# Kernel optimization log

Hardware: AMD Instinct MI355X
Metric: run time of the kernel (lower is better)

The kernel has to match this reference:

```python
import jax, jax.numpy as jnp
import numpy as np

N_NODES = 50000
N_EDGES = 800000
N_GRAPHS = 256
HEADS = 4
OUT_CH = 32
HIDDEN = HEADS * OUT_CH  # 128
NUM_LAYERS = 3
NEG_SLOPE = 0.2
BN_EPS = 1e-5


def setup_inputs() -> dict:
    key = jax.random.key(0)
    ks = jax.random.split(key, 12)
    x = jax.random.normal(ks[0], (N_NODES, HIDDEN), dtype=jnp.float32)
    edge_index = jax.random.randint(ks[1], (2, N_EDGES), 0, N_NODES, dtype=jnp.int64)
    batch = jnp.sort(jax.random.randint(ks[2], (N_NODES,), 0, N_GRAPHS, dtype=jnp.int64))
    s = 1.0 / np.sqrt(HIDDEN)
    W = jax.random.normal(ks[3], (NUM_LAYERS, HIDDEN, HIDDEN), dtype=jnp.float32) * s
    att_src = jax.random.normal(ks[4], (NUM_LAYERS, HEADS, OUT_CH), dtype=jnp.float32) * s
    att_dst = jax.random.normal(ks[5], (NUM_LAYERS, HEADS, OUT_CH), dtype=jnp.float32) * s
    bias = jnp.zeros((NUM_LAYERS, HIDDEN), dtype=jnp.float32)
    bn_gamma = jnp.ones((NUM_LAYERS, HIDDEN), dtype=jnp.float32)
    bn_beta = jnp.zeros((NUM_LAYERS, HIDDEN), dtype=jnp.float32)
    bn_mean = jnp.zeros((NUM_LAYERS, HIDDEN), dtype=jnp.float32)
    bn_var = jnp.ones((NUM_LAYERS, HIDDEN), dtype=jnp.float32)
    fc1_w = jax.random.normal(ks[6], (HIDDEN, HIDDEN // 2), dtype=jnp.float32) * s
    fc1_b = jnp.zeros((HIDDEN // 2,), dtype=jnp.float32)
    fc2_w = jax.random.normal(ks[7], (HIDDEN // 2, 10), dtype=jnp.float32) * (1.0 / np.sqrt(HIDDEN // 2))
    fc2_b = jnp.zeros((10,), dtype=jnp.float32)
    return {"x": x, "edge_index": edge_index, "batch": batch, "W": W,
            "att_src": att_src, "att_dst": att_dst, "bias": bias,
            "bn_gamma": bn_gamma, "bn_beta": bn_beta, "bn_mean": bn_mean,
            "bn_var": bn_var, "fc1_w": fc1_w, "fc1_b": fc1_b,
            "fc2_w": fc2_w, "fc2_b": fc2_b}


def _gat_layer(x, src, dst, W, a_src, a_dst, b):
    n = x.shape[0]
    h = (x @ W).reshape(n, HEADS, OUT_CH)                       # [N,H,C]
    alpha_s = jnp.einsum('nhc,hc->nh', h, a_src)                # [N,H]
    alpha_d = jnp.einsum('nhc,hc->nh', h, a_dst)                # [N,H]
    score = jax.nn.leaky_relu(alpha_s[src] + alpha_d[dst], NEG_SLOPE)  # [E,H]
    # segment softmax over destination node (self-loops guarantee nonempty segments)
    m = jax.lax.stop_gradient(jax.ops.segment_max(score, dst, num_segments=n))
    e = jnp.exp(score - m[dst])
    denom = jax.ops.segment_sum(e, dst, num_segments=n)
    alpha = e / denom[dst]                                      # [E,H]
    msg = h[src] * alpha[:, :, None]                            # [E,H,C]
    out = jax.ops.segment_sum(msg, dst, num_segments=n)         # [N,H,C]
    return out.reshape(n, HEADS * OUT_CH) + b


def reference(x, edge_index, batch, W, att_src, att_dst, bias,
              bn_gamma, bn_beta, bn_mean, bn_var,
              fc1_w, fc1_b, fc2_w, fc2_b):
    n = x.shape[0]
    loop = jnp.arange(n, dtype=edge_index.dtype)
    src = jnp.concatenate([edge_index[0], loop])  # add self-loops (PyG default)
    dst = jnp.concatenate([edge_index[1], loop])
    for i in range(NUM_LAYERS):
        x = _gat_layer(x, src, dst, W[i], att_src[i], att_dst[i], bias[i])
        x = (x - bn_mean[i]) * (bn_gamma[i] / jnp.sqrt(bn_var[i] + BN_EPS)) + bn_beta[i]
        x = jax.nn.elu(x)
    # global mean pool over graphs
    sums = jax.ops.segment_sum(x, batch, num_segments=N_GRAPHS)
    cnts = jax.ops.segment_sum(jnp.ones((n,), dtype=x.dtype), batch, num_segments=N_GRAPHS)
    pooled = sums / jnp.maximum(cnts, 1.0)[:, None]
    hmid = jax.nn.relu(pooled @ fc1_w + fc1_b)
    logits = hmid @ fc2_w + fc2_b
    return logits
```

## Files before the change

kernel.cpp:

```cpp
#include <hip/hip_runtime.h>
#include <hip/hip_fp16.h>
#include <math.h>

#define N_NODES 50000
#define N_EDGES 800000
#define E_TOTAL (N_EDGES + N_NODES)
#define N_GRAPHS 256
#define HEADS 4
#define OUT_CH 32
#define HIDDEN 128
#define NUM_LAYERS 3
#define NEG_SLOPE 0.2f
#define BN_EPS 1e-5f
#define NBLK_SCAN ((N_NODES + 255) / 256)


__global__ void zero_kernel(unsigned int* __restrict__ p, int n) {
    int i = blockIdx.x * blockDim.x + threadIdx.x;
    if (i < n) p[i] = 0u;
}


__global__ void hist_kernel(const int* __restrict__ dst, int* __restrict__ deg,
                            int* __restrict__ rank) {
    int e = blockIdx.x * blockDim.x + threadIdx.x;
    if (e >= E_TOTAL) return;
    int d = (e < N_EDGES) ? dst[e] : (e - N_EDGES);
    rank[e] = atomicAdd(&deg[d], 1);
}

__global__ __launch_bounds__(256) void scan1_kernel(const int* __restrict__ deg,
                                                    int* __restrict__ rowoff,
                                                    int* __restrict__ bsum, int n) {
    int i = blockIdx.x * 256 + threadIdx.x;
    int v = (i < n) ? deg[i] : 0;
    int lane = threadIdx.x & 63, wv = threadIdx.x >> 6;
    int s = v;
    for (int off = 1; off < 64; off <<= 1) {
        int u = __shfl_up(s, off);
        if (lane >= off) s += u;
    }
    __shared__ int wtot[4];
    if (lane == 63) wtot[wv] = s;
    __syncthreads();
    int add = 0;
    for (int w = 0; w < wv; ++w) add += wtot[w];
    s += add;
    if (i < n) rowoff[i + 1] = s;
    if (threadIdx.x == 255) bsum[blockIdx.x] = s;
}

__global__ __launch_bounds__(256) void scan2_kernel(int* __restrict__ bsum, int nb) {
    int t = threadIdx.x;
    int v = (t < nb) ? bsum[t] : 0;
    int lane = t & 63, wv = t >> 6;
    int s = v;
    for (int off = 1; off < 64; off <<= 1) {
        int u = __shfl_up(s, off);
        if (lane >= off) s += u;
    }
    __shared__ int wtot[4];
    if (lane == 63) wtot[wv] = s;
    __syncthreads();
    int add = 0;
    for (int w = 0; w < wv; ++w) add += wtot[w];
    s += add;
    if (t < nb) bsum[t] = s - v;
}

__global__ __launch_bounds__(256) void scan3_kernel(const int* __restrict__ bsum,
                                                    int* __restrict__ rowoff, int n) {
    int i = blockIdx.x * 256 + threadIdx.x;
    if (i == 0) rowoff[0] = 0;
    if (i < n) rowoff[i + 1] += bsum[blockIdx.x];
}

__global__ void scatter_kernel(const int* __restrict__ src, const int* __restrict__ dst,
                               const int* __restrict__ rowoff, const int* __restrict__ rank,
                               int2* __restrict__ edgebuf) {
    int e = blockIdx.x * blockDim.x + threadIdx.x;
    if (e >= E_TOTAL) return;
    int s, d;
    if (e < N_EDGES) { s = src[e]; d = dst[e]; }
    else             { s = e - N_EDGES; d = s; }
    int pos = rowoff[d] + rank[e];
    edgebuf[pos] = make_int2(s, d);
}


__global__ __launch_bounds__(256) void gemm_xw(const float* __restrict__ X,
                                               const float* __restrict__ W,
                                               const float* __restrict__ att_src,
                                               const float* __restrict__ att_dst,
                                               __half* __restrict__ Hh,
                                               float* __restrict__ as4,
                                               float* __restrict__ ad4, int n) {
    __shared__ float xst[32][36];
    __shared__ float ws[32][128];
    const int row0 = blockIdx.x * 32;
    const int cg = threadIdx.x & 31;
    const int rg = threadIdx.x >> 5;
    float acc[4][4];
#pragma unroll
    for (int r = 0; r < 4; ++r)
#pragma unroll
        for (int j = 0; j < 4; ++j) acc[r][j] = 0.f;

    for (int k0 = 0; k0 < 128; k0 += 32) {
        {
            int r = threadIdx.x >> 3;
            int kk = (threadIdx.x & 7) * 4;
            int swz = (kk >> 2) & 7;
            int cswz = (((r >> 2) ^ swz) << 2) | (r & 3);
            int gr = row0 + r;
            float4 v = make_float4(0.f, 0.f, 0.f, 0.f);
            if (gr < n) v = *reinterpret_cast<const float4*>(&X[gr * 128 + k0 + kk]);
            xst[kk + 0][cswz] = v.x; xst[kk + 1][cswz] = v.y;
            xst[kk + 2][cswz] = v.z; xst[kk + 3][cswz] = v.w;
        }
        for (int i = threadIdx.x; i < 32 * 128 / 4; i += 256) {
            int p = i * 4;
            int kk = p >> 7, cc = p & 127;
            *reinterpret_cast<float4*>(&ws[kk][cc]) =
                *reinterpret_cast<const float4*>(&W[(k0 + kk) * 128 + cc]);
        }
        __syncthreads();
#pragma unroll
        for (int kk = 0; kk < 32; ++kk) {
            const int swz = (kk >> 2) & 7;
            float4 wv = *reinterpret_cast<const float4*>(&ws[kk][cg * 4]);
            float4 xv = *reinterpret_cast<const float4*>(&xst[kk][((rg ^ swz) << 2)]);
            acc[0][0] += xv.x * wv.x; acc[0][1] += xv.x * wv.y; acc[0][2] += xv.x * wv.z; acc[0][3] += xv.x * wv.w;
            acc[1][0] += xv.y * wv.x; acc[1][1] += xv.y * wv.y; acc[1][2] += xv.y * wv.z; acc[1][3] += xv.y * wv.w;
            acc[2][0] += xv.z * wv.x; acc[2][1] += xv.z * wv.y; acc[2][2] += xv.z * wv.z; acc[2][3] += xv.z * wv.w;
            acc[3][0] += xv.w * wv.x; acc[3][1] += xv.w * wv.y; acc[3][2] += xv.w * wv.z; acc[3][3] += xv.w * wv.w;
        }
        __syncthreads();
    }

#pragma unroll
    for (int r = 0; r < 4; ++r) {
        int gr = row0 + rg * 4 + r;
        if (gr < n) {
            __half2 ab = __floats2half2_rn(acc[r][0], acc[r][1]);
            __half2 cd = __floats2half2_rn(acc[r][2], acc[r][3]);
            uint2 u;
            u.x = *reinterpret_cast<unsigned*>(&ab);
            u.y = *reinterpret_cast<unsigned*>(&cd);
            *reinterpret_cast<uint2*>(&Hh[(size_t)gr * 128 + cg * 4]) = u;
        }
    }

    const int h = cg >> 3;
    const int co = (cg & 7) * 4;
    float4 asw = *reinterpret_cast<const float4*>(att_src + h * OUT_CH + co);
    float4 adw = *reinterpret_cast<const float4*>(att_dst + h * OUT_CH + co);
#pragma unroll
    for (int r = 0; r < 4; ++r) {
        float s = acc[r][0] * asw.x + acc[r][1] * asw.y + acc[r][2] * asw.z + acc[r][3] * asw.w;
        float d = acc[r][0] * adw.x + acc[r][1] * adw.y + acc[r][2] * adw.z + acc[r][3] * adw.w;
        s += __shfl_xor(s, 1); d += __shfl_xor(d, 1);
        s += __shfl_xor(s, 2); d += __shfl_xor(d, 2);
        s += __shfl_xor(s, 4); d += __shfl_xor(d, 4);
        if ((cg & 7) == 0) {
            int gr = row0 + rg * 4 + r;
            if (gr < n) {
                as4[gr * 4 + h] = s;
                ad4[gr * 4 + h] = d;
            }
        }
    }
}


__global__ __launch_bounds__(256) void escore_kernel(const int2* __restrict__ edgebuf,
                                                     const float* __restrict__ as4,
                                                     const float* __restrict__ ad4,
                                                     float* __restrict__ esc) {
    int j = blockIdx.x * blockDim.x + threadIdx.x;
    if (j >= E_TOTAL) return;
    int2 ed = edgebuf[j];
    float4 a = *reinterpret_cast<const float4*>(&as4[ed.x * 4]);
    float4 b = *reinterpret_cast<const float4*>(&ad4[ed.y * 4]);
    float x0 = a.x + b.x, x1 = a.y + b.y, x2 = a.z + b.z, x3 = a.w + b.w;
    x0 = x0 > 0.f ? x0 : x0 * NEG_SLOPE;
    x1 = x1 > 0.f ? x1 : x1 * NEG_SLOPE;
    x2 = x2 > 0.f ? x2 : x2 * NEG_SLOPE;
    x3 = x3 > 0.f ? x3 : x3 * NEG_SLOPE;
    float4 e = make_float4(__expf(x0), __expf(x1), __expf(x2), __expf(x3));
    *reinterpret_cast<float4*>(&esc[(size_t)j * 4]) = e;
}


template <int USE_ESC>
__global__ __launch_bounds__(256) void aggregate_kernel(
    const __half2* __restrict__ Hh2, const float* __restrict__ as4, const float* __restrict__ ad4,
    const float* __restrict__ esc,
    const int* __restrict__ rowoff, const int2* __restrict__ edgebuf,
    const float* __restrict__ bias, const float* __restrict__ gamma, const float* __restrict__ beta,
    const float* __restrict__ mean, const float* __restrict__ var,
    float* __restrict__ Xout, int n) {
    int wid = (blockIdx.x * blockDim.x + threadIdx.x) >> 6;
    if (wid >= n) return;
    int lane = threadIdx.x & 63;
    int hd = lane >> 4;
    int c = lane * 2;

    float adv = USE_ESC ? 0.f : ad4[wid * 4 + hd];

    int jbeg = rowoff[wid], jend = rowoff[wid + 1];

    float s = 0.f, ax = 0.f, ay = 0.f;

    for (int base = jbeg; base < jend; base += 64) {
        int myj = base + lane;
        int mysrc = (myj < jend) ? edgebuf[myj].x : 0;
        int cnt = min(64, jend - base);
        int t = 0;
        if (USE_ESC) {
#pragma unroll 1
            for (; t + 8 <= cnt; t += 8) {
                int s0 = __shfl(mysrc, t + 0);
                int s1 = __shfl(mysrc, t + 1);
                int s2 = __shfl(mysrc, t + 2);
                int s3 = __shfl(mysrc, t + 3);
                int s4 = __shfl(mysrc, t + 4);
                int s5 = __shfl(mysrc, t + 5);
                int s6 = __shfl(mysrc, t + 6);
                int s7 = __shfl(mysrc, t + 7);
                float e0 = esc[(size_t)(base + t + 0) * 4 + hd];
                float e1 = esc[(size_t)(base + t + 1) * 4 + hd];
                float e2 = esc[(size_t)(base + t + 2) * 4 + hd];
                float e3 = esc[(size_t)(base + t + 3) * 4 + hd];
                float e4 = esc[(size_t)(base + t + 4) * 4 + hd];
                float e5 = esc[(size_t)(base + t + 5) * 4 + hd];
                float e6 = esc[(size_t)(base + t + 6) * 4 + hd];
                float e7 = esc[(size_t)(base + t + 7) * 4 + hd];
                float2 h0 = __half22float2(Hh2[(size_t)s0 * 64 + lane]);
                float2 h1 = __half22float2(Hh2[(size_t)s1 * 64 + lane]);
                float2 h2 = __half22float2(Hh2[(size_t)s2 * 64 + lane]);
                float2 h3 = __half22float2(Hh2[(size_t)s3 * 64 + lane]);
                float2 h4 = __half22float2(Hh2[(size_t)s4 * 64 + lane]);
                float2 h5 = __half22float2(Hh2[(size_t)s5 * 64 + lane]);
                float2 h6 = __half22float2(Hh2[(size_t)s6 * 64 + lane]);
                float2 h7 = __half22float2(Hh2[(size_t)s7 * 64 + lane]);
                s  += ((e0 + e1) + (e2 + e3)) + ((e4 + e5) + (e6 + e7));
                ax += e0 * h0.x + e1 * h1.x + e2 * h2.x + e3 * h3.x
                    + e4 * h4.x + e5 * h5.x + e6 * h6.x + e7 * h7.x;
                ay += e0 * h0.y + e1 * h1.y + e2 * h2.y + e3 * h3.y
                    + e4 * h4.y + e5 * h5.y + e6 * h6.y + e7 * h7.y;
            }
        }
        for (; t < cnt; ++t) {
            int src = __shfl(mysrc, t);
            float e;
            if (USE_ESC) {
                e = esc[(size_t)(base + t) * 4 + hd];
            } else {
                float sc = as4[src * 4 + hd] + adv;
                sc = sc > 0.f ? sc : sc * NEG_SLOPE;
                e = __expf(sc);
            }
            float2 hv = __half22float2(Hh2[(size_t)src * 64 + lane]);
            s += e;
            ax += e * hv.x;
            ay += e * hv.y;
        }
    }

    float inv = 1.f / s;
    float v0 = ax * inv + bias[c];
    float v1 = ay * inv + bias[c + 1];
    v0 = (v0 - mean[c])     * (gamma[c]     * rsqrtf(var[c]     + BN_EPS)) + beta[c];
    v1 = (v1 - mean[c + 1]) * (gamma[c + 1] * rsqrtf(var[c + 1] + BN_EPS)) + beta[c + 1];
    v0 = v0 > 0.f ? v0 : expm1f(v0);
    v1 = v1 > 0.f ? v1 : expm1f(v1);
    float2 o = make_float2(v0, v1);
    *reinterpret_cast<float2*>(&Xout[(size_t)wid * HIDDEN + c]) = o;
}


__global__ __launch_bounds__(1024) void pool_fc_kernel(
    const float* __restrict__ X, const int* __restrict__ batch,
    const float* __restrict__ fc1w, const float* __restrict__ fc1b,
    const float* __restrict__ fc2w, const float* __restrict__ fc2b,
    float* __restrict__ out) {
    int g = blockIdx.x;
    int tid = threadIdx.x;
    int cg = (tid & 31) * 4;
    int rg = tid >> 5;

    int lo = 0, hi = N_NODES;
    while (lo < hi) { int mid = (lo + hi) >> 1; if (batch[mid] < g) lo = mid + 1; else hi = mid; }
    int lo2 = lo, hi2 = N_NODES;
    while (lo2 < hi2) { int mid = (lo2 + hi2) >> 1; if (batch[mid] < g + 1) lo2 = mid + 1; else hi2 = mid; }

    float ax = 0.f, ay = 0.f, az = 0.f, aw = 0.f;
    for (int i = lo + rg; i < lo2; i += 32) {
        float4 v = *reinterpret_cast<const float4*>(&X[(size_t)i * HIDDEN + cg]);
        ax += v.x; ay += v.y; az += v.z; aw += v.w;
    }

    __shared__ float red[32][132];
    red[rg][cg + 0] = ax; red[rg][cg + 1] = ay;
    red[rg][cg + 2] = az; red[rg][cg + 3] = aw;
    __syncthreads();
#pragma unroll
    for (int step = 16; step >= 1; step >>= 1) {
        if (rg < step) {
            red[rg][cg + 0] += red[rg + step][cg + 0];
            red[rg][cg + 1] += red[rg + step][cg + 1];
            red[rg][cg + 2] += red[rg + step][cg + 2];
            red[rg][cg + 3] += red[rg + step][cg + 3];
        }
        __syncthreads();
    }

    __shared__ float pooled[HIDDEN];
    __shared__ float hmid[64];
    if (rg == 0) {
        float inv = 1.f / fmaxf((float)(lo2 - lo), 1.0f);
        pooled[cg + 0] = red[0][cg + 0] * inv;
        pooled[cg + 1] = red[0][cg + 1] * inv;
        pooled[cg + 2] = red[0][cg + 2] * inv;
        pooled[cg + 3] = red[0][cg + 3] * inv;
    }
    __syncthreads();
    if (tid < 64) {
        float a = fc1b[tid];
#pragma unroll 8
        for (int k = 0; k < 128; ++k) a += pooled[k] * fc1w[k * 64 + tid];
        hmid[tid] = fmaxf(a, 0.f);
    }
    __syncthreads();
    if (tid < 10) {
        float a = fc2b[tid];
#pragma unroll 8
        for (int k = 0; k < 64; ++k) a += hmid[k] * fc2w[k * 10 + tid];
        out[g * 10 + tid] = a;
    }
}


static inline size_t align_up(size_t x, size_t a) { return (x + a - 1) & ~(a - 1); }

extern "C" void kernel_launch(void* const* d_in, const int* in_sizes, int n_in,
                              void* d_out, int out_size, void* d_ws, size_t ws_size,
                              hipStream_t stream) {
    const float* x        = (const float*)d_in[0];
    const int*   eidx     = (const int*)d_in[1];
    const int*   batch    = (const int*)d_in[2];
    const float* W        = (const float*)d_in[3];
    const float* att_src  = (const float*)d_in[4];
    const float* att_dst  = (const float*)d_in[5];
    const float* bias     = (const float*)d_in[6];
    const float* bn_gamma = (const float*)d_in[7];
    const float* bn_beta  = (const float*)d_in[8];
    const float* bn_mean  = (const float*)d_in[9];
    const float* bn_var   = (const float*)d_in[10];
    const float* fc1w     = (const float*)d_in[11];
    const float* fc1b     = (const float*)d_in[12];
    const float* fc2w     = (const float*)d_in[13];
    const float* fc2b     = (const float*)d_in[14];
    float* out = (float*)d_out;

    const int* src = eidx;
    const int* dst = eidx + N_EDGES;

    char* p = (char*)d_ws;
    size_t off = 0;
    auto alloc = [&](size_t bytes) {
        size_t o = off;
        off = align_up(off + bytes, 256);
        return (void*)(p + o);
    };
    __half* Hh     = (__half*)alloc((size_t)N_NODES * HIDDEN * 2);
    float* Xbuf    = (float*)alloc((size_t)N_NODES * HIDDEN * 4);
    float* as4     = (float*)alloc((size_t)N_NODES * HEADS * 4);
    float* ad4     = (float*)alloc((size_t)N_NODES * HEADS * 4);
    int*   deg     = (int*)alloc((size_t)N_NODES * 4);
    int*   rowoff  = (int*)alloc((size_t)(N_NODES + 1) * 4);
    int*   rank    = (int*)alloc((size_t)E_TOTAL * 4);
    int*   bsum    = (int*)alloc((size_t)NBLK_SCAN * 4);
    int2*  edgebuf = (int2*)alloc((size_t)E_TOTAL * 8);
    float* esc     = (float*)alloc((size_t)E_TOTAL * HEADS * 4);
    const bool use_esc = (off <= ws_size);
    (void)n_in; (void)in_sizes; (void)out_size;

    zero_kernel<<<(N_NODES + 255) / 256, 256, 0, stream>>>((unsigned int*)deg, N_NODES);

    hist_kernel<<<(E_TOTAL + 255) / 256, 256, 0, stream>>>(dst, deg, rank);
    scan1_kernel<<<NBLK_SCAN, 256, 0, stream>>>(deg, rowoff, bsum, N_NODES);
    scan2_kernel<<<1, 256, 0, stream>>>(bsum, NBLK_SCAN);
    scan3_kernel<<<NBLK_SCAN, 256, 0, stream>>>(bsum, rowoff, N_NODES);
    scatter_kernel<<<(E_TOTAL + 255) / 256, 256, 0, stream>>>(src, dst, rowoff, rank, edgebuf);

    const float* xcur = x;
    for (int layer = 0; layer < NUM_LAYERS; ++layer) {
        const float* Wl  = W + (size_t)layer * HIDDEN * HIDDEN;
        const float* asl = att_src + (size_t)layer * HEADS * OUT_CH;
        const float* adl = att_dst + (size_t)layer * HEADS * OUT_CH;
        const float* bl  = bias + (size_t)layer * HIDDEN;
        const float* gl  = bn_gamma + (size_t)layer * HIDDEN;
        const float* btl = bn_beta + (size_t)layer * HIDDEN;
        const float* ml  = bn_mean + (size_t)layer * HIDDEN;
        const float* vl  = bn_var + (size_t)layer * HIDDEN;

        gemm_xw<<<(N_NODES + 31) / 32, 256, 0, stream>>>(xcur, Wl, asl, adl, Hh, as4, ad4, N_NODES);
        if (use_esc) {
            escore_kernel<<<(E_TOTAL + 255) / 256, 256, 0, stream>>>(edgebuf, as4, ad4, esc);
            aggregate_kernel<1><<<(N_NODES * 64 + 255) / 256, 256, 0, stream>>>(
                (const __half2*)Hh, as4, ad4, esc, rowoff, edgebuf, bl, gl, btl, ml, vl, Xbuf, N_NODES);
        } else {
            aggregate_kernel<0><<<(N_NODES * 64 + 255) / 256, 256, 0, stream>>>(
                (const __half2*)Hh, as4, ad4, esc, rowoff, edgebuf, bl, gl, btl, ml, vl, Xbuf, N_NODES);
        }
        xcur = Xbuf;
    }

    pool_fc_kernel<<<N_GRAPHS, 1024, 0, stream>>>(xcur, batch, fc1w, fc1b, fc2w, fc2b, out);
}
```

Baseline: 402.3 us.

## Fuse edge score computation into aggregation and store only source indices in CSR

Removes the separate per-layer escore kernel and its E×4 float buffer. Attention weights are now recomputed inside the aggregation loop from gathered as4 values, using an 8-wide unrolled path. The CSR edge buffer shrinks from int2 (src,dst) to int src only. This cuts global memory traffic and one launch per layer, at the cost of an extra gather from as4 and more exp work inside the aggregation kernel.

```diff
diff --git a/kernel.cpp b/kernel.cpp
--- a/kernel.cpp
+++ b/kernel.cpp
@@ -77,14 +77,14 @@
 
 __global__ void scatter_kernel(const int* __restrict__ src, const int* __restrict__ dst,
                                const int* __restrict__ rowoff, const int* __restrict__ rank,
-                               int2* __restrict__ edgebuf) {
+                               int* __restrict__ col) {
     int e = blockIdx.x * blockDim.x + threadIdx.x;
     if (e >= E_TOTAL) return;
     int s, d;
     if (e < N_EDGES) { s = src[e]; d = dst[e]; }
     else             { s = e - N_EDGES; d = s; }
     int pos = rowoff[d] + rank[e];
-    edgebuf[pos] = make_int2(s, d);
+    col[pos] = s;
 }
 
 
@@ -173,30 +173,9 @@
 }
 
 
-__global__ __launch_bounds__(256) void escore_kernel(const int2* __restrict__ edgebuf,
-                                                     const float* __restrict__ as4,
-                                                     const float* __restrict__ ad4,
-                                                     float* __restrict__ esc) {
-    int j = blockIdx.x * blockDim.x + threadIdx.x;
-    if (j >= E_TOTAL) return;
-    int2 ed = edgebuf[j];
-    float4 a = *reinterpret_cast<const float4*>(&as4[ed.x * 4]);
-    float4 b = *reinterpret_cast<const float4*>(&ad4[ed.y * 4]);
-    float x0 = a.x + b.x, x1 = a.y + b.y, x2 = a.z + b.z, x3 = a.w + b.w;
-    x0 = x0 > 0.f ? x0 : x0 * NEG_SLOPE;
-    x1 = x1 > 0.f ? x1 : x1 * NEG_SLOPE;
-    x2 = x2 > 0.f ? x2 : x2 * NEG_SLOPE;
-    x3 = x3 > 0.f ? x3 : x3 * NEG_SLOPE;
-    float4 e = make_float4(__expf(x0), __expf(x1), __expf(x2), __expf(x3));
-    *reinterpret_cast<float4*>(&esc[(size_t)j * 4]) = e;
-}
-
-
-template <int USE_ESC>
 __global__ __launch_bounds__(256) void aggregate_kernel(
     const __half2* __restrict__ Hh2, const float* __restrict__ as4, const float* __restrict__ ad4,
-    const float* __restrict__ esc,
-    const int* __restrict__ rowoff, const int2* __restrict__ edgebuf,
+    const int* __restrict__ rowoff, const int* __restrict__ col,
     const float* __restrict__ bias, const float* __restrict__ gamma, const float* __restrict__ beta,
     const float* __restrict__ mean, const float* __restrict__ var,
     float* __restrict__ Xout, int n) {
@@ -206,7 +185,7 @@
     int hd = lane >> 4;
     int c = lane * 2;
 
-    float adv = USE_ESC ? 0.f : ad4[wid * 4 + hd];
+    float adv = ad4[wid * 4 + hd];
 
     int jbeg = rowoff[wid], jend = rowoff[wid + 1];
 
@@ -214,53 +193,62 @@
 
     for (int base = jbeg; base < jend; base += 64) {
         int myj = base + lane;
-        int mysrc = (myj < jend) ? edgebuf[myj].x : 0;
+        int mysrc = (myj < jend) ? col[myj] : 0;
         int cnt = min(64, jend - base);
         int t = 0;
-        if (USE_ESC) {
 #pragma unroll 1
-            for (; t + 8 <= cnt; t += 8) {
-                int s0 = __shfl(mysrc, t + 0);
-                int s1 = __shfl(mysrc, t + 1);
-                int s2 = __shfl(mysrc, t + 2);
-                int s3 = __shfl(mysrc, t + 3);
-                int s4 = __shfl(mysrc, t + 4);
-                int s5 = __shfl(mysrc, t + 5);
-                int s6 = __shfl(mysrc, t + 6);
-                int s7 = __shfl(mysrc, t + 7);
-                float e0 = esc[(size_t)(base + t + 0) * 4 + hd];
-                float e1 = esc[(size_t)(base + t + 1) * 4 + hd];
-                float e2 = esc[(size_t)(base + t + 2) * 4 + hd];
-                float e3 = esc[(size_t)(base + t + 3) * 4 + hd];
-                float e4 = esc[(size_t)(base + t + 4) * 4 + hd];
-                float e5 = esc[(size_t)(base + t + 5) * 4 + hd];
-                float e6 = esc[(size_t)(base + t + 6) * 4 + hd];
-                float e7 = esc[(size_t)(base + t + 7) * 4 + hd];
-                float2 h0 = __half22float2(Hh2[(size_t)s0 * 64 + lane]);
-                float2 h1 = __half22float2(Hh2[(size_t)s1 * 64 + lane]);
-                float2 h2 = __half22float2(Hh2[(size_t)s2 * 64 + lane]);
-                float2 h3 = __half22float2(Hh2[(size_t)s3 * 64 + lane]);
-                float2 h4 = __half22float2(Hh2[(size_t)s4 * 64 + lane]);
-                float2 h5 = __half22float2(Hh2[(size_t)s5 * 64 + lane]);
-                float2 h6 = __half22float2(Hh2[(size_t)s6 * 64 + lane]);
-                float2 h7 = __half22float2(Hh2[(size_t)s7 * 64 + lane]);
-                s  += ((e0 + e1) + (e2 + e3)) + ((e4 + e5) + (e6 + e7));
-                ax += e0 * h0.x + e1 * h1.x + e2 * h2.x + e3 * h3.x
-                    + e4 * h4.x + e5 * h5.x + e6 * h6.x + e7 * h7.x;
-                ay += e0 * h0.y + e1 * h1.y + e2 * h2.y + e3 * h3.y
-                    + e4 * h4.y + e5 * h5.y + e6 * h6.y + e7 * h7.y;
-            }
+        for (; t + 8 <= cnt; t += 8) {
+            int s0 = __shfl(mysrc, t + 0);
+            int s1 = __shfl(mysrc, t + 1);
+            int s2 = __shfl(mysrc, t + 2);
+            int s3 = __shfl(mysrc, t + 3);
+            int s4 = __shfl(mysrc, t + 4);
+            int s5 = __shfl(mysrc, t + 5);
+            int s6 = __shfl(mysrc, t + 6);
+            int s7 = __shfl(mysrc, t + 7);
+            float a0 = as4[s0 * 4 + hd];
+            float a1 = as4[s1 * 4 + hd];
+            float a2 = as4[s2 * 4 + hd];
+            float a3 = as4[s3 * 4 + hd];
+            float a4 = as4[s4 * 4 + hd];
+            float a5 = as4[s5 * 4 + hd];
+            float a6 = as4[s6 * 4 + hd];
+            float a7 = as4[s7 * 4 + hd];
+            float2 h0 = __half22float2(Hh2[(size_t)s0 * 64 + lane]);
+            float2 h1 = __half22float2(Hh2[(size_t)s1 * 64 + lane]);
+            float2 h2 = __half22float2(Hh2[(size_t)s2 * 64 + lane]);
+            float2 h3 = __half22float2(Hh2[(size_t)s3 * 64 + lane]);
+            float2 h4 = __half22float2(Hh2[(size_t)s4 * 64 + lane]);
+            float2 h5 = __half22float2(Hh2[(size_t)s5 * 64 + lane]);
+            float2 h6 = __half22float2(Hh2[(size_t)s6 * 64 + lane]);
+            float2 h7 = __half22float2(Hh2[(size_t)s7 * 64 + lane]);
+            float x0 = a0 + adv; x0 = x0 > 0.f ? x0 : x0 * NEG_SLOPE;
+            float x1 = a1 + adv; x1 = x1 > 0.f ? x1 : x1 * NEG_SLOPE;
+            float x2 = a2 + adv; x2 = x2 > 0.f ? x2 : x2 * NEG_SLOPE;
+            float x3 = a3 + adv; x3 = x3 > 0.f ? x3 : x3 * NEG_SLOPE;
+            float x4 = a4 + adv; x4 = x4 > 0.f ? x4 : x4 * NEG_SLOPE;
+            float x5 = a5 + adv; x5 = x5 > 0.f ? x5 : x5 * NEG_SLOPE;
+            float x6 = a6 + adv; x6 = x6 > 0.f ? x6 : x6 * NEG_SLOPE;
+            float x7 = a7 + adv; x7 = x7 > 0.f ? x7 : x7 * NEG_SLOPE;
+            float e0 = __expf(x0);
+            float e1 = __expf(x1);
+            float e2 = __expf(x2);
+            float e3 = __expf(x3);
+            float e4 = __expf(x4);
+            float e5 = __expf(x5);
+            float e6 = __expf(x6);
+            float e7 = __expf(x7);
+            s  += ((e0 + e1) + (e2 + e3)) + ((e4 + e5) + (e6 + e7));
+            ax += e0 * h0.x + e1 * h1.x + e2 * h2.x + e3 * h3.x
+                + e4 * h4.x + e5 * h5.x + e6 * h6.x + e7 * h7.x;
+            ay += e0 * h0.y + e1 * h1.y + e2 * h2.y + e3 * h3.y
+                + e4 * h4.y + e5 * h5.y + e6 * h6.y + e7 * h7.y;
         }
         for (; t < cnt; ++t) {
             int src = __shfl(mysrc, t);
-            float e;
-            if (USE_ESC) {
-                e = esc[(size_t)(base + t) * 4 + hd];
-            } else {
-                float sc = as4[src * 4 + hd] + adv;
-                sc = sc > 0.f ? sc : sc * NEG_SLOPE;
-                e = __expf(sc);
-            }
+            float sc = as4[src * 4 + hd] + adv;
+            sc = sc > 0.f ? sc : sc * NEG_SLOPE;
+            float e = __expf(sc);
             float2 hv = __half22float2(Hh2[(size_t)src * 64 + lane]);
             s += e;
             ax += e * hv.x;
@@ -382,10 +370,8 @@
     int*   rowoff  = (int*)alloc((size_t)(N_NODES + 1) * 4);
     int*   rank    = (int*)alloc((size_t)E_TOTAL * 4);
     int*   bsum    = (int*)alloc((size_t)NBLK_SCAN * 4);
-    int2*  edgebuf = (int2*)alloc((size_t)E_TOTAL * 8);
-    float* esc     = (float*)alloc((size_t)E_TOTAL * HEADS * 4);
-    const bool use_esc = (off <= ws_size);
-    (void)n_in; (void)in_sizes; (void)out_size;
+    int*   col     = (int*)alloc((size_t)E_TOTAL * 4);
+    (void)n_in; (void)in_sizes; (void)out_size; (void)ws_size;
 
     zero_kernel<<<(N_NODES + 255) / 256, 256, 0, stream>>>((unsigned int*)deg, N_NODES);
 
@@ -393,7 +379,7 @@
     scan1_kernel<<<NBLK_SCAN, 256, 0, stream>>>(deg, rowoff, bsum, N_NODES);
     scan2_kernel<<<1, 256, 0, stream>>>(bsum, NBLK_SCAN);
     scan3_kernel<<<NBLK_SCAN, 256, 0, stream>>>(bsum, rowoff, N_NODES);
-    scatter_kernel<<<(E_TOTAL + 255) / 256, 256, 0, stream>>>(src, dst, rowoff, rank, edgebuf);
+    scatter_kernel<<<(E_TOTAL + 255) / 256, 256, 0, stream>>>(src, dst, rowoff, rank, col);
 
     const float* xcur = x;
     for (int layer = 0; layer < NUM_LAYERS; ++layer) {
@@ -407,14 +393,8 @@
         const float* vl  = bn_var + (size_t)layer * HIDDEN;
 
         gemm_xw<<<(N_NODES + 31) / 32, 256, 0, stream>>>(xcur, Wl, asl, adl, Hh, as4, ad4, N_NODES);
-        if (use_esc) {
-            escore_kernel<<<(E_TOTAL + 255) / 256, 256, 0, stream>>>(edgebuf, as4, ad4, esc);
-            aggregate_kernel<1><<<(N_NODES * 64 + 255) / 256, 256, 0, stream>>>(
-                (const __half2*)Hh, as4, ad4, esc, rowoff, edgebuf, bl, gl, btl, ml, vl, Xbuf, N_NODES);
-        } else {
-            aggregate_kernel<0><<<(N_NODES * 64 + 255) / 256, 256, 0, stream>>>(
-                (const __half2*)Hh, as4, ad4, esc, rowoff, edgebuf, bl, gl, btl, ml, vl, Xbuf, N_NODES);
-        }
+        aggregate_kernel<<<(N_NODES * 64 + 255) / 256, 256, 0, stream>>>(
+            (const __half2*)Hh, as4, ad4, rowoff, col, bl, gl, btl, ml, vl, Xbuf, N_NODES);
         xcur = Xbuf;
     }
 
```

Result: faster. 383.8 us (-4.6%).
